# Kernel optimization log

Hardware: AMD Instinct MI355X
Metric: run time of the kernel (lower is better)

The kernel has to match this reference:

```python
import jax, jax.numpy as jnp
import numpy as np

COMMITMENT_COST = 0.25


def setup_inputs() -> dict:
    key = jax.random.key(0)
    k1, k2 = jax.random.split(key)
    inputs = jax.random.normal(k1, (32, 64, 32, 32), dtype=jnp.float32)  # (B, C, H, W)
    embed = jax.random.normal(k2, (64, 1024), dtype=jnp.float32)          # (embedding_dim, num_embeddings)
    return {"inputs": inputs, "embed": embed}


def reference(inputs, embed):
    # Eval-mode forward (EMA buffer updates are training-only side effects).
    B, C, H, W = inputs.shape
    K = embed.shape[1]
    flat = inputs.transpose(0, 2, 3, 1).reshape(-1, C)  # (N, C)
    N = flat.shape[0]

    distances = (jnp.sum(flat * flat, axis=1, keepdims=True)
                 + jnp.sum(embed * embed, axis=0)
                 - 2.0 * flat @ embed)
    encoding_indices = jnp.argmin(distances, axis=1)  # (N,)

    # Gather instead of one-hot @ embed.T (same math, no N x K one-hot)
    quantized = embed.T[encoding_indices]  # (N, C)

    e_latent_loss = jnp.mean((jax.lax.stop_gradient(quantized) - flat) ** 2)
    loss = COMMITMENT_COST * e_latent_loss

    # straight-through estimator
    quantized_st = flat + jax.lax.stop_gradient(quantized - flat)
    quantized_out = quantized_st.reshape(B, H, W, C).transpose(0, 3, 1, 2)

    # avg_probs via scatter-add counts (== mean of one-hot encodings)
    counts = jnp.zeros((K,), dtype=flat.dtype).at[encoding_indices].add(1.0)
    avg_probs = counts / N
    perplexity = jnp.exp(-jnp.sum(avg_probs * jnp.log(avg_probs + 1e-10)))

    return quantized_out, loss, encoding_indices, perplexity
```

## Files before the change

kernel.cpp:

```cpp
#include <hip/hip_runtime.h>

#define N_PIX  32768
#define C_DIM  64
#define K_EMB  1024
#define HW     1024
#define PIXB   64

#define OUT_Q_OFF    0
#define OUT_LOSS_OFF 2097152
#define OUT_IDX_OFF  2097153
#define OUT_PERP_OFF 2129921

typedef __attribute__((ext_vector_type(8)))  __bf16 bf16x8;
typedef __attribute__((ext_vector_type(16))) float  f32x16;

__device__ unsigned short g_esplit[3 * K_EMB * C_DIM];
__device__ float          g_ee[K_EMB];
__device__ unsigned int   g_counts[K_EMB];
__device__ float          g_lossAcc;

__device__ __forceinline__ unsigned short f2bf(float f) {
    unsigned u = __float_as_uint(f);
    unsigned r = u + 0x7FFFu + ((u >> 16) & 1u);
    return (unsigned short)(r >> 16);
}
__device__ __forceinline__ float bf2f(unsigned short b) {
    return __uint_as_float(((unsigned)b) << 16);
}
__device__ __forceinline__ unsigned long long pack_score(float d, int k) {
    unsigned int u = __float_as_uint(d);
    u = (u & 0x80000000u) ? ~u : (u | 0x80000000u);
    return ((unsigned long long)u << 32) | (unsigned int)k;
}
__device__ __forceinline__ uint4 pack8(const unsigned short* v) {
    uint4 u;
    u.x = (unsigned)v[0] | ((unsigned)v[1] << 16);
    u.y = (unsigned)v[2] | ((unsigned)v[3] << 16);
    u.z = (unsigned)v[4] | ((unsigned)v[5] << 16);
    u.w = (unsigned)v[6] | ((unsigned)v[7] << 16);
    return u;
}
__device__ __forceinline__ unsigned long long shfl_xor32_u64(unsigned long long v) {
    unsigned lo = (unsigned)v, hi = (unsigned)(v >> 32);
    lo = __shfl_xor(lo, 32, 64);
    hi = __shfl_xor(hi, 32, 64);
    return ((unsigned long long)hi << 32) | lo;
}
#define UPD2(P1, P2, MM) { \
    if ((MM) < P1) { P2 = P1; P1 = (MM); } else if ((MM) < P2) P2 = (MM); }
#define MRG2(P1, P2, O1, O2) { \
    unsigned long long _lo = (O1) < P1 ? (O1) : P1; \
    unsigned long long _hi = (O1) < P1 ? P1 : (O1); \
    unsigned long long _m2 = (O2) < P2 ? (O2) : P2; \
    P1 = _lo; P2 = _hi < _m2 ? _hi : _m2; }

__global__ void k_prep(const float* __restrict__ embed) {
    const int code = blockIdx.x * 64 + threadIdx.x;
    if (code == 0) g_lossAcc = 0.f;
    g_counts[code] = 0u;
    const int tile = code >> 5, c32 = code & 31;
    float ee = 0.f;
#pragma unroll 8
    for (int c = 0; c < C_DIM; ++c) {
        const float x = embed[c * K_EMB + code];
        ee = fmaf(x, x, ee);
        const unsigned short b1 = f2bf(x);
        const float r1 = x - bf2f(b1);
        const unsigned short b2 = f2bf(r1);
        const float r2 = r1 - bf2f(b2);
        const unsigned short b3 = f2bf(r2);
        const int s = c >> 4, hh = (c >> 3) & 1, e = c & 7;
        const int rest = ((((tile * 4 + s) * 2 + hh) * 32) + c32) * 8 + e;
        g_esplit[rest          ] = b1;
        g_esplit[rest +  65536 ] = b2;
        g_esplit[rest + 131072 ] = b3;
    }
    g_ee[code] = ee;
}

__global__ __launch_bounds__(256, 2) void k_main(
    const float* __restrict__ inp, const float* __restrict__ embed,
    float* __restrict__ out_q, float* __restrict__ out_idx) {

    __shared__ float x_raw[C_DIM * PIXB];
    __shared__ uint4 xfrag[3 * 4 * 2 * PIXB];
    __shared__ unsigned long long red1[4][PIXB];
    __shared__ unsigned long long red2[4][PIXB];
    __shared__ int   ksel[PIXB];
    __shared__ float lred[4];
    __shared__ float bdist;

    const int tid = threadIdx.x;
    const int n0  = blockIdx.x * PIXB;
    const int b   = n0 >> 10;
    const int hw0 = n0 & 1023;
    const float* __restrict__ xg = inp + b * (C_DIM * HW) + hw0;

#pragma unroll
    for (int i = 0; i < 4; ++i) {
        const int F = tid + i * 256;
        const int c = F >> 4, p4 = (F & 15) << 2;
        *reinterpret_cast<float4*>(&x_raw[F << 2]) =
            *reinterpret_cast<const float4*>(xg + c * HW + p4);
    }
    __syncthreads();

    float sx2 = 0.f;
#pragma unroll
    for (int cc = 0; cc < 2; ++cc) {
        const int cid = tid + cc * 256;
        const int s = cid >> 7, hh = (cid >> 6) & 1, p = cid & 63;
        unsigned short b1[8], b2[8], b3[8];
#pragma unroll
        for (int e = 0; e < 8; ++e) {
            const float x = x_raw[(s * 16 + hh * 8 + e) * PIXB + p];
            sx2 = fmaf(x, x, sx2);
            b1[e] = f2bf(x);
            const float r1 = x - bf2f(b1[e]);
            b2[e] = f2bf(r1);
            const float r2 = r1 - bf2f(b2[e]);
            b3[e] = f2bf(r2);
        }
        const int fi = (s * 2 + hh) * PIXB + p;
        xfrag[fi            ] = pack8(b1);
        xfrag[fi + 8 * PIXB ] = pack8(b2);
        xfrag[fi + 16 * PIXB] = pack8(b3);
    }
    for (int off = 32; off; off >>= 1) sx2 += __shfl_down(sx2, off, 64);
    if ((tid & 63) == 0) lred[tid >> 6] = sx2;
    __syncthreads();

    const int w   = tid >> 6;
    const int ln  = tid & 63;
    const int c31 = ln & 31;
    const int h   = ln >> 5;
    const uint4* __restrict__ eg = reinterpret_cast<const uint4*>(g_esplit);

    unsigned long long p1a = ~0ull, p2a = ~0ull;
    unsigned long long p1b = ~0ull, p2b = ~0ull;

#pragma unroll 1
    for (int r = 0; r < 8; ++r) {
        const int ct = r * 4 + w;
        const int cb = ct * 32;

        uint4 ae[3][4];
#pragma unroll
        for (int j = 0; j < 3; ++j)
#pragma unroll
            for (int s = 0; s < 4; ++s)
                ae[j][s] = eg[(((j * 32 + ct) * 4 + s) * 2 + h) * 32 + c31];

        float eev[16];
#pragma unroll
        for (int rg = 0; rg < 16; ++rg)
            eev[rg] = g_ee[cb + (rg & 3) + 8 * (rg >> 2) + 4 * h];

#pragma unroll
        for (int pt = 0; pt < 2; ++pt) {
            const int pbase = pt * 32 + c31;
            f32x16 acc = {};
#pragma unroll
            for (int ib = 0; ib < 3; ++ib) {
                uint4 bx[4];
#pragma unroll
                for (int s = 0; s < 4; ++s)
                    bx[s] = xfrag[(ib * 8 + s * 2 + h) * PIXB + pbase];
#pragma unroll
                for (int ja = 0; ja < 3 - ib; ++ja)
#pragma unroll
                    for (int s = 0; s < 4; ++s)
                        acc = __builtin_amdgcn_mfma_f32_32x32x16_bf16(
                            __builtin_bit_cast(bf16x8, ae[ja][s]),
                            __builtin_bit_cast(bf16x8, bx[s]),
                            acc, 0, 0, 0);
            }
#pragma unroll
            for (int rg = 0; rg < 16; ++rg) {
                const float dist = fmaf(-2.f, acc[rg], eev[rg]);
                const unsigned long long mm =
                    pack_score(dist, cb + (rg & 3) + 8 * (rg >> 2) + 4 * h);
                if (pt == 0) { UPD2(p1a, p2a, mm) }
                else         { UPD2(p1b, p2b, mm) }
            }
        }
    }

    {
        unsigned long long o1 = shfl_xor32_u64(p1a), o2 = shfl_xor32_u64(p2a);
        MRG2(p1a, p2a, o1, o2)
        o1 = shfl_xor32_u64(p1b); o2 = shfl_xor32_u64(p2b);
        MRG2(p1b, p2b, o1, o2)
        if (ln < 32) {
            red1[w][ln] = p1a; red2[w][ln] = p2a;
            red1[w][ln + 32] = p1b; red2[w][ln + 32] = p2b;
        }
    }
    __syncthreads();

    if (tid < PIXB) {
        unsigned long long M1 = red1[0][tid], M2 = red2[0][tid];
        MRG2(M1, M2, red1[1][tid], red2[1][tid])
        MRG2(M1, M2, red1[2][tid], red2[2][tid])
        MRG2(M1, M2, red1[3][tid], red2[3][tid])
        const int k1 = (int)(unsigned int)(M1 & 0xFFFFFFFFull);
        const int k2 = (int)(unsigned int)(M2 & 0xFFFFFFFFull);
        float d1 = 0.f, d2 = 0.f;
        const float* xcol = x_raw + tid;
#pragma unroll 8
        for (int c = 0; c < C_DIM; ++c) {
            const float xv = xcol[c * PIXB];
            d1 = fmaf(xv, embed[c * K_EMB + k1], d1);
            d2 = fmaf(xv, embed[c * K_EMB + k2], d2);
        }
        const float dist1 = fmaf(-2.f, d1, g_ee[k1]);
        const float dist2 = fmaf(-2.f, d2, g_ee[k2]);
        const unsigned long long s1 = pack_score(dist1, k1);
        const unsigned long long s2 = pack_score(dist2, k2);
        const unsigned long long m = s1 < s2 ? s1 : s2;
        const int k = (int)(unsigned int)(m & 0xFFFFFFFFull);
        ksel[tid] = k;
        out_idx[n0 + tid] = (float)k;
        atomicAdd(g_counts + k, 1u);
        const unsigned int u = (unsigned int)(m >> 32);
        float dist = __uint_as_float((u & 0x80000000u) ? (u & 0x7FFFFFFFu) : ~u);
        for (int off = 32; off; off >>= 1) dist += __shfl_down(dist, off, 64);
        if (tid == 0) bdist = dist;
    }
    __syncthreads();

    {
        const int c  = tid >> 2;
        const int p0 = (tid & 3) * 16;
        float* oq = out_q + b * (C_DIM * HW) + c * HW + hw0 + p0;
        const float* er = embed + c * K_EMB;
#pragma unroll
        for (int i = 0; i < 4; ++i) {
            float4 q;
            q.x = er[ksel[p0 + i * 4 + 0]];
            q.y = er[ksel[p0 + i * 4 + 1]];
            q.z = er[ksel[p0 + i * 4 + 2]];
            q.w = er[ksel[p0 + i * 4 + 3]];
            *reinterpret_cast<float4*>(oq + i * 4) = q;
        }
    }
    if (tid == 0)
        atomicAdd(&g_lossAcc, lred[0] + lred[1] + lred[2] + lred[3] + bdist);
}

__global__ __launch_bounds__(1024) void k_scalar(float* __restrict__ out_loss,
                                                 float* __restrict__ out_perp) {
    __shared__ float red[16];
    const int tid = threadIdx.x;
    float p = (float)g_counts[tid] * (1.0f / (float)N_PIX);
    float t = p * logf(p + 1e-10f);
    for (int off = 32; off; off >>= 1) t += __shfl_down(t, off, 64);
    if ((tid & 63) == 0) red[tid >> 6] = t;
    __syncthreads();
    if (tid == 0) {
        float s = 0.f;
#pragma unroll
        for (int i = 0; i < 16; ++i) s += red[i];
        *out_perp = expf(-s);
        *out_loss = 0.25f * g_lossAcc * (1.0f / (float)(N_PIX * C_DIM));
    }
}

extern "C" void kernel_launch(void* const* d_in, const int* in_sizes, int n_in,
                              void* d_out, int out_size, void* d_ws, size_t ws_size,
                              hipStream_t stream) {
    const float* inp   = (const float*)d_in[0];
    const float* embed = (const float*)d_in[1];
    float* out = (float*)d_out;

    k_prep<<<dim3(16), dim3(64), 0, stream>>>(embed);
    k_main<<<dim3(N_PIX / PIXB), dim3(256), 0, stream>>>(
        inp, embed, out + OUT_Q_OFF, out + OUT_IDX_OFF);
    k_scalar<<<dim3(1), dim3(1024), 0, stream>>>(out + OUT_LOSS_OFF,
                                                 out + OUT_PERP_OFF);
}
```

Baseline: 117.0 us.

## Fold codebook norm into MFMA and double-buffer codebook fragment loads

The codebook squared norm, scaled by -0.5, is split into three bf16 parts and folded into the GEMM as an extra MFMA against a ones vector. This removes the per-tile g_ee loads and the FMA epilogue. Codebook fragments for the next tile are prefetched into a second register set while the current tile computes, and the first tile's loads are issued before the input staging. The prep kernel now writes packed uint4 fragments instead of scalar shorts. The trade-off is higher register pressure and one extra MFMA per tile.

After: 136.5 us. 16.6% more time.

```diff
diff --git a/kernel.cpp b/kernel.cpp
--- a/kernel.cpp
+++ b/kernel.cpp
@@ -15,6 +15,7 @@
 typedef __attribute__((ext_vector_type(16))) float  f32x16;
 
 __device__ unsigned short g_esplit[3 * K_EMB * C_DIM];
+__device__ uint4          g_eesplit[2 * K_EMB];
 __device__ float          g_ee[K_EMB];
 __device__ unsigned int   g_counts[K_EMB];
 __device__ float          g_lossAcc;
@@ -59,23 +60,38 @@
     if (code == 0) g_lossAcc = 0.f;
     g_counts[code] = 0u;
     const int tile = code >> 5, c32 = code & 31;
+    uint4* o = reinterpret_cast<uint4*>(g_esplit);
     float ee = 0.f;
-#pragma unroll 8
-    for (int c = 0; c < C_DIM; ++c) {
-        const float x = embed[c * K_EMB + code];
-        ee = fmaf(x, x, ee);
-        const unsigned short b1 = f2bf(x);
-        const float r1 = x - bf2f(b1);
-        const unsigned short b2 = f2bf(r1);
-        const float r2 = r1 - bf2f(b2);
-        const unsigned short b3 = f2bf(r2);
-        const int s = c >> 4, hh = (c >> 3) & 1, e = c & 7;
-        const int rest = ((((tile * 4 + s) * 2 + hh) * 32) + c32) * 8 + e;
-        g_esplit[rest          ] = b1;
-        g_esplit[rest +  65536 ] = b2;
-        g_esplit[rest + 131072 ] = b3;
-    }
+#pragma unroll
+    for (int s = 0; s < 4; ++s)
+#pragma unroll
+        for (int hh = 0; hh < 2; ++hh) {
+            unsigned short b1[8], b2[8], b3[8];
+#pragma unroll
+            for (int e = 0; e < 8; ++e) {
+                const float x = embed[(s * 16 + hh * 8 + e) * K_EMB + code];
+                ee = fmaf(x, x, ee);
+                b1[e] = f2bf(x);
+                const float r1 = x - bf2f(b1[e]);
+                b2[e] = f2bf(r1);
+                const float r2 = r1 - bf2f(b2[e]);
+                b3[e] = f2bf(r2);
+            }
+            const int oi = tile * 256 + s * 64 + hh * 32 + c32;
+            o[oi        ] = pack8(b1);
+            o[oi +  8192] = pack8(b2);
+            o[oi + 16384] = pack8(b3);
+        }
     g_ee[code] = ee;
+    const float v = -0.5f * ee;
+    const unsigned short e1 = f2bf(v);
+    const float r1 = v - bf2f(e1);
+    const unsigned short e2 = f2bf(r1);
+    const float r2 = r1 - bf2f(e2);
+    const unsigned short e3 = f2bf(r2);
+    g_eesplit[code] = make_uint4((unsigned)e1 | ((unsigned)e2 << 16),
+                                 (unsigned)e3, 0u, 0u);
+    g_eesplit[K_EMB + code] = make_uint4(0u, 0u, 0u, 0u);
 }
 
 __global__ __launch_bounds__(256, 2) void k_main(
@@ -95,6 +111,21 @@
     const int b   = n0 >> 10;
     const int hw0 = n0 & 1023;
     const float* __restrict__ xg = inp + b * (C_DIM * HW) + hw0;
+
+    const int w   = tid >> 6;
+    const int ln  = tid & 63;
+    const int c31 = ln & 31;
+    const int h   = ln >> 5;
+    const uint4* __restrict__ eg = reinterpret_cast<const uint4*>(g_esplit);
+    const int abase = h * 32 + c31;
+
+    uint4 pA[8], pAe, pB[8], pBe;
+    {
+        const int b0 = w * 256 + abase;
+#pragma unroll
+        for (int s = 0; s < 4; ++s) { pA[s] = eg[b0 + s * 64]; pA[4 + s] = eg[b0 + 8192 + s * 64]; }
+        pAe = g_eesplit[h * K_EMB + w * 32 + c31];
+    }
 
 #pragma unroll
     for (int i = 0; i < 4; ++i) {
@@ -130,61 +161,53 @@
     if ((tid & 63) == 0) lred[tid >> 6] = sx2;
     __syncthreads();
 
-    const int w   = tid >> 6;
-    const int ln  = tid & 63;
-    const int c31 = ln & 31;
-    const int h   = ln >> 5;
-    const uint4* __restrict__ eg = reinterpret_cast<const uint4*>(g_esplit);
-
     unsigned long long p1a = ~0ull, p2a = ~0ull;
     unsigned long long p1b = ~0ull, p2b = ~0ull;
+    const uint4 bones = make_uint4(h ? 0u : 0x3F803F80u, h ? 0u : 0x00003F80u, 0u, 0u);
+
+#define MFMA1(AF, BF) \
+    acc = __builtin_amdgcn_mfma_f32_32x32x16_bf16( \
+        __builtin_bit_cast(bf16x8, AF), __builtin_bit_cast(bf16x8, BF), acc, 0, 0, 0);
+
+#define STEP(CUR, CURE, NXT, NXTE, R) { \
+    const int ct = (R) * 4 + w; \
+    const int b0 = ct * 256 + abase; \
+    uint4 a2[4]; \
+    _Pragma("unroll") for (int s = 0; s < 4; ++s) a2[s] = eg[b0 + 16384 + s * 64]; \
+    { const int rn = (R) < 7 ? (R) + 1 : 7; \
+      const int bn = (rn * 4 + w) * 256 + abase; \
+      _Pragma("unroll") for (int s = 0; s < 4; ++s) { \
+          NXT[s] = eg[bn + s * 64]; NXT[4 + s] = eg[bn + 8192 + s * 64]; } \
+      NXTE = g_eesplit[h * K_EMB + (rn * 4 + w) * 32 + c31]; } \
+    const int cb = ct * 32; \
+    _Pragma("unroll") for (int pt = 0; pt < 2; ++pt) { \
+        const int pbase = pt * 32 + c31; \
+        f32x16 acc = {}; \
+        MFMA1(CURE, bones) \
+        uint4 bx0[4], bx1[4], bx2[4]; \
+        _Pragma("unroll") for (int s = 0; s < 4; ++s) bx0[s] = xfrag[(     s * 2 + h) * PIXB + pbase]; \
+        _Pragma("unroll") for (int s = 0; s < 4; ++s) { MFMA1(CUR[s], bx0[s]) }       \
+        _Pragma("unroll") for (int s = 0; s < 4; ++s) { MFMA1(CUR[4 + s], bx0[s]) }   \
+        _Pragma("unroll") for (int s = 0; s < 4; ++s) bx1[s] = xfrag[( 8 + s * 2 + h) * PIXB + pbase]; \
+        _Pragma("unroll") for (int s = 0; s < 4; ++s) { MFMA1(CUR[s], bx1[s]) }       \
+        _Pragma("unroll") for (int s = 0; s < 4; ++s) { MFMA1(CUR[4 + s], bx1[s]) }   \
+        _Pragma("unroll") for (int s = 0; s < 4; ++s) bx2[s] = xfrag[(16 + s * 2 + h) * PIXB + pbase]; \
+        _Pragma("unroll") for (int s = 0; s < 4; ++s) { MFMA1(CUR[s], bx2[s]) }       \
+        _Pragma("unroll") for (int s = 0; s < 4; ++s) { MFMA1(a2[s], bx0[s]) }        \
+        _Pragma("unroll") for (int rg = 0; rg < 16; ++rg) { \
+            const unsigned long long mm = \
+                pack_score(-acc[rg], cb + (rg & 3) + 8 * (rg >> 2) + 4 * h); \
+            if (pt == 0) { UPD2(p1a, p2a, mm) } else { UPD2(p1b, p2b, mm) } \
+        } \
+    } }
 
 #pragma unroll 1
-    for (int r = 0; r < 8; ++r) {
-        const int ct = r * 4 + w;
-        const int cb = ct * 32;
-
-        uint4 ae[3][4];
-#pragma unroll
-        for (int j = 0; j < 3; ++j)
-#pragma unroll
-            for (int s = 0; s < 4; ++s)
-                ae[j][s] = eg[(((j * 32 + ct) * 4 + s) * 2 + h) * 32 + c31];
-
-        float eev[16];
-#pragma unroll
-        for (int rg = 0; rg < 16; ++rg)
-            eev[rg] = g_ee[cb + (rg & 3) + 8 * (rg >> 2) + 4 * h];
-
-#pragma unroll
-        for (int pt = 0; pt < 2; ++pt) {
-            const int pbase = pt * 32 + c31;
-            f32x16 acc = {};
-#pragma unroll
-            for (int ib = 0; ib < 3; ++ib) {
-                uint4 bx[4];
-#pragma unroll
-                for (int s = 0; s < 4; ++s)
-                    bx[s] = xfrag[(ib * 8 + s * 2 + h) * PIXB + pbase];
-#pragma unroll
-                for (int ja = 0; ja < 3 - ib; ++ja)
-#pragma unroll
-                    for (int s = 0; s < 4; ++s)
-                        acc = __builtin_amdgcn_mfma_f32_32x32x16_bf16(
-                            __builtin_bit_cast(bf16x8, ae[ja][s]),
-                            __builtin_bit_cast(bf16x8, bx[s]),
-                            acc, 0, 0, 0);
-            }
-#pragma unroll
-            for (int rg = 0; rg < 16; ++rg) {
-                const float dist = fmaf(-2.f, acc[rg], eev[rg]);
-                const unsigned long long mm =
-                    pack_score(dist, cb + (rg & 3) + 8 * (rg >> 2) + 4 * h);
-                if (pt == 0) { UPD2(p1a, p2a, mm) }
-                else         { UPD2(p1b, p2b, mm) }
-            }
-        }
-    }
+    for (int rr = 0; rr < 4; ++rr) {
+        STEP(pA, pAe, pB, pBe, 2 * rr)
+        STEP(pB, pBe, pA, pAe, 2 * rr + 1)
+    }
+#undef STEP
+#undef MFMA1
 
     {
         unsigned long long o1 = shfl_xor32_u64(p1a), o2 = shfl_xor32_u64(p2a);
@@ -217,13 +240,12 @@
         const float dist2 = fmaf(-2.f, d2, g_ee[k2]);
         const unsigned long long s1 = pack_score(dist1, k1);
         const unsigned long long s2 = pack_score(dist2, k2);
-        const unsigned long long m = s1 < s2 ? s1 : s2;
-        const int k = (int)(unsigned int)(m & 0xFFFFFFFFull);
+        const int  k     = (s1 < s2) ? k1 : k2;
+        const float distw = (s1 < s2) ? dist1 : dist2;
         ksel[tid] = k;
         out_idx[n0 + tid] = (float)k;
         atomicAdd(g_counts + k, 1u);
-        const unsigned int u = (unsigned int)(m >> 32);
-        float dist = __uint_as_float((u & 0x80000000u) ? (u & 0x7FFFFFFFu) : ~u);
+        float dist = distw;
         for (int off = 32; off; off >>= 1) dist += __shfl_down(dist, off, 64);
         if (tid == 0) bdist = dist;
     }
```
